# Optimization experiments

Measured on AMD Instinct MI355X. Metric: run time of the kernel, lower is better.

The kernel has to match this reference:

```python
import jax, jax.numpy as jnp
import numpy as np
from jax import lax


def _conv2d(x, w, b, stride):
    # x: [B,C,H,W], w: [O,I,kh,kw], b: [O]
    y = lax.conv_general_dilated(
        x, w, window_strides=(stride, stride), padding='VALID',
        dimension_numbers=('NCHW', 'OIHW', 'NCHW'))
    return y + b[None, :, None, None]


def setup_inputs() -> dict:
    key = jax.random.key(0)
    ks = jax.random.split(key, 4)
    B, C, H, W = 8, 128, 128, 128
    x = jax.random.normal(ks[0], (B, C, H, W), dtype=jnp.float32)
    # conv weights, scaled like torch default init (~1/sqrt(fan_in))
    Wq = jax.random.normal(ks[1], (C, C, 2, 2), dtype=jnp.float32) / np.sqrt(C * 4)
    Wk = jax.random.normal(ks[2], (C, C, 2, 2), dtype=jnp.float32) / np.sqrt(C * 4)
    Wv = jax.random.normal(ks[3], (C, C, 1, 1), dtype=jnp.float32) / np.sqrt(C)
    bq = jnp.zeros((C,), dtype=jnp.float32)
    bk = jnp.zeros((C,), dtype=jnp.float32)
    bv = jnp.zeros((C,), dtype=jnp.float32)
    return {'x': x, 'Wq': Wq, 'bq': bq, 'Wk': Wk, 'bk': bk, 'Wv': Wv, 'bv': bv}


def reference(x, Wq, bq, Wk, bk, Wv, bv):
    B, C, H, W = x.shape
    # query/key: 2x2 stride-2 convs -> [B, C, (H//2)*(W//2)]
    q = _conv2d(x, Wq, bq, 2).reshape(B, C, -1)
    k = _conv2d(x, Wk, bk, 2).reshape(B, C, -1)
    # value: 1x1 conv -> [B, C, H*W]
    v = _conv2d(x, Wv, bv, 1).reshape(B, C, -1)
    # energy: [B, C, C]
    energy = jnp.einsum('bcn,bdn->bcd', q, k)
    # max-subtract trick: softmax over (row_max - energy)
    energy_new = jnp.max(energy, axis=-1, keepdims=True) - energy
    attention = jax.nn.softmax(energy_new, axis=-1)
    out = jnp.einsum('bcd,bdn->bcn', attention, v)
    return out.reshape(B, C, H, W)
```

## Files before the change

kernel.cpp:

```cpp
#include <hip/hip_runtime.h>
#include <math.h>


typedef float f32x4 __attribute__((ext_vector_type(4)));
typedef short s16x8 __attribute__((ext_vector_type(8)));

__device__ __forceinline__ unsigned short f2bf(float f) {
  union { float f; unsigned u; } v; v.f = f;
  unsigned r = v.u + 0x7FFFu + ((v.u >> 16) & 1u);
  return (unsigned short)(r >> 16);
}
__device__ __forceinline__ float bf2f(unsigned short h) {
  union { unsigned u; float f; } v; v.u = ((unsigned)h) << 16;
  return v.f;
}
__device__ __forceinline__ unsigned pack2(unsigned short a, unsigned short b) {
  return (unsigned)a | ((unsigned)b << 16);
}

__global__ __launch_bounds__(256) void k_prep(
    const float* __restrict__ Wq, const float* __restrict__ Wk,
    unsigned short* __restrict__ Wth, unsigned short* __restrict__ Wtl) {
  const int f = (blockIdx.x * 256 + threadIdx.x) * 4;
  const int row = f >> 9;
  const int k   = f & 511;
  const float* src = (row < 128) ? &Wq[row * 512 + k] : &Wk[(row - 128) * 512 + k];
  float4 v = *(const float4*)src;
  unsigned short h0 = f2bf(v.x), h1 = f2bf(v.y), h2 = f2bf(v.z), h3 = f2bf(v.w);
  unsigned short l0 = f2bf(v.x - bf2f(h0)), l1 = f2bf(v.y - bf2f(h1));
  unsigned short l2 = f2bf(v.z - bf2f(h2)), l3 = f2bf(v.w - bf2f(h3));
  const int di = (k >> 5) * 8192 + row * 32 + (k & 31);
  *(ushort4*)&Wth[di] = make_ushort4(h0, h1, h2, h3);
  *(ushort4*)&Wtl[di] = make_ushort4(l0, l1, l2, l3);
}

__global__ __launch_bounds__(256, 3) void k_conv_energy(
    const float* __restrict__ x,
    const unsigned short* __restrict__ Wth, const unsigned short* __restrict__ Wtl,
    const float* __restrict__ bq, const float* __restrict__ bk,
    float* __restrict__ epart) {
  __shared__ unsigned short LDS[16384];
  unsigned short* Th = LDS;
  unsigned short* Tl = LDS + 8192;

  const int t = threadIdx.x;
  const int nt = blockIdx.x, b = blockIdx.y;
  const int w = t >> 6, lane = t & 63;
  const int lrow = lane & 15, lkb = lane >> 4;

  const int pp = t >> 4;
  const int ci_l = pp >> 1, kh = pp & 1;
  const int i16 = t & 15;
  const int klb = ci_l * 4 + kh * 2;
  const float* xb = x + ((size_t)b << 21);
  const float* xrow = xb + (size_t)ci_l * 16384 + (2 * nt + kh) * 128 + 2 * i16;

  f32x4 acc[4][4];
#pragma unroll
  for (int m = 0; m < 4; ++m)
#pragma unroll
    for (int n = 0; n < 4; ++n) acc[m][n] = (f32x4){0.f, 0.f, 0.f, 0.f};

  s16x8 pfh[4], pfl[4];
  float2 pv[2][4];
  const int aoff = (w * 64 + lrow) * 32 + lkb * 8;

#pragma unroll
  for (int m = 0; m < 4; ++m) {
    pfh[m] = *(const s16x8*)&Wth[aoff + m * 512];
    pfl[m] = *(const s16x8*)&Wtl[aoff + m * 512];
  }
  {
    float2 v0 = *(const float2*)&xrow[0];
    float2 v1 = *(const float2*)&xrow[32];
    float2 v2 = *(const float2*)&xrow[64];
    float2 v3 = *(const float2*)&xrow[96];
    unsigned short hx, hy;
    hx = f2bf(v0.x); hy = f2bf(v0.y);
    *(unsigned*)&LDS[(i16     ) * 40 + klb] = pack2(hx, hy);
    *(unsigned*)&LDS[2560 + (i16     ) * 40 + klb] = pack2(f2bf(v0.x - bf2f(hx)), f2bf(v0.y - bf2f(hy)));
    hx = f2bf(v1.x); hy = f2bf(v1.y);
    *(unsigned*)&LDS[(i16 + 16) * 40 + klb] = pack2(hx, hy);
    *(unsigned*)&LDS[2560 + (i16 + 16) * 40 + klb] = pack2(f2bf(v1.x - bf2f(hx)), f2bf(v1.y - bf2f(hy)));
    hx = f2bf(v2.x); hy = f2bf(v2.y);
    *(unsigned*)&LDS[(i16 + 32) * 40 + klb] = pack2(hx, hy);
    *(unsigned*)&LDS[2560 + (i16 + 32) * 40 + klb] = pack2(f2bf(v2.x - bf2f(hx)), f2bf(v2.y - bf2f(hy)));
    hx = f2bf(v3.x); hy = f2bf(v3.y);
    *(unsigned*)&LDS[(i16 + 48) * 40 + klb] = pack2(hx, hy);
    *(unsigned*)&LDS[2560 + (i16 + 48) * 40 + klb] = pack2(f2bf(v3.x - bf2f(hx)), f2bf(v3.y - bf2f(hy)));
  }
#pragma unroll
  for (int g = 0; g < 4; ++g)
    pv[1][g] = *(const float2*)&xrow[(size_t)8 * 16384 + 32 * g];
  __syncthreads();

#pragma unroll
  for (int step = 0; step < 16; ++step) {
    const int cur = step & 1;
    const unsigned short* Bh = LDS + cur * 5120;
    const unsigned short* Bl = Bh + 2560;
    s16x8 bfh[4], bfl[4];
#pragma unroll
    for (int nf = 0; nf < 4; ++nf) {
      const int bidx = (nf * 16 + lrow) * 40 + lkb * 8;
      bfh[nf] = *(const s16x8*)&Bh[bidx];
      bfl[nf] = *(const s16x8*)&Bl[bidx];
    }
#pragma unroll
    for (int m = 0; m < 4; ++m)
#pragma unroll
      for (int n = 0; n < 4; ++n) {
        acc[m][n] = __builtin_amdgcn_mfma_f32_16x16x32_bf16(pfh[m], bfh[n], acc[m][n], 0, 0, 0);
        acc[m][n] = __builtin_amdgcn_mfma_f32_16x16x32_bf16(pfh[m], bfl[n], acc[m][n], 0, 0, 0);
        acc[m][n] = __builtin_amdgcn_mfma_f32_16x16x32_bf16(pfl[m], bfh[n], acc[m][n], 0, 0, 0);
      }
    if (step < 15) {
      const unsigned short* Wh_n = Wth + (step + 1) * 8192;
      const unsigned short* Wl_n = Wtl + (step + 1) * 8192;
#pragma unroll
      for (int m = 0; m < 4; ++m) {
        pfh[m] = *(const s16x8*)&Wh_n[aoff + m * 512];
        pfl[m] = *(const s16x8*)&Wl_n[aoff + m * 512];
      }
    }
    if (step < 14) {
#pragma unroll
      for (int g = 0; g < 4; ++g)
        pv[cur][g] = *(const float2*)&xrow[(size_t)(step + 2) * 8 * 16384 + 32 * g];
    }
    if (step < 15) {
      unsigned short* Nh = LDS + (cur ^ 1) * 5120;
      unsigned short* Nl = Nh + 2560;
#pragma unroll
      for (int g = 0; g < 4; ++g) {
        const int n = i16 + 16 * g;
        unsigned short hx = f2bf(pv[cur ^ 1][g].x), hy = f2bf(pv[cur ^ 1][g].y);
        *(unsigned*)&Nh[n * 40 + klb] = pack2(hx, hy);
        *(unsigned*)&Nl[n * 40 + klb] = pack2(f2bf(pv[cur ^ 1][g].x - bf2f(hx)),
                                              f2bf(pv[cur ^ 1][g].y - bf2f(hy)));
      }
      asm volatile("s_waitcnt lgkmcnt(0)" ::: "memory");
      __builtin_amdgcn_s_barrier();
    }
  }
  __syncthreads();

  const float* biasp = (w < 2) ? bq : bk;
  const int rb = (w & 1) * 64;
  float biasr[16];
#pragma unroll
  for (int m = 0; m < 4; ++m)
#pragma unroll
    for (int i = 0; i < 4; ++i)
      biasr[m * 4 + i] = biasp[rb + m * 16 + (lane >> 4) * 4 + i];

  f32x4 e[4][4];
#pragma unroll
  for (int m = 0; m < 4; ++m)
#pragma unroll
    for (int n = 0; n < 4; ++n) e[m][n] = (f32x4){0.f, 0.f, 0.f, 0.f};

  const int mrow0 = (w >> 1) * 64;
  const int nrow0 = 128 + (w & 1) * 64;

#pragma unroll
  for (int ks = 0; ks < 2; ++ks) {
#pragma unroll
    for (int m = 0; m < 4; ++m) {
      const int r0 = w * 64 + m * 16 + (lane >> 4) * 4;
#pragma unroll
      for (int nn = 0; nn < 2; ++nn) {
        const int n = 2 * ks + nn;
        const int cl = nn * 16 + lrow;
        const int cl8 = cl >> 3, c7 = cl & 7;
#pragma unroll
        for (int i = 0; i < 4; ++i) {
          const int r = r0 + i;
          const float vv = acc[m][n][i] + biasr[m * 4 + i];
          const unsigned short h = f2bf(vv);
          const unsigned short l = f2bf(vv - bf2f(h));
          const int ad = r * 32 + ((cl8 ^ (r & 3)) << 3) + c7;
          Th[ad] = h;
          Tl[ad] = l;
        }
      }
    }
    __syncthreads();
    {
      s16x8 qh[4], ql[4], kh8[4], kl8[4];
#pragma unroll
      for (int m = 0; m < 4; ++m) {
        const int r = mrow0 + m * 16 + lrow;
        const int ad = r * 32 + ((lkb ^ (r & 3)) << 3);
        qh[m] = *(const s16x8*)&Th[ad];
        ql[m] = *(const s16x8*)&Tl[ad];
      }
#pragma unroll
      for (int n = 0; n < 4; ++n) {
        const int r = nrow0 + n * 16 + lrow;
        const int ad = r * 32 + ((lkb ^ (r & 3)) << 3);
        kh8[n] = *(const s16x8*)&Th[ad];
        kl8[n] = *(const s16x8*)&Tl[ad];
      }
#pragma unroll
      for (int m = 0; m < 4; ++m)
#pragma unroll
        for (int n = 0; n < 4; ++n) {
          e[m][n] = __builtin_amdgcn_mfma_f32_16x16x32_bf16(qh[m], kh8[n], e[m][n], 0, 0, 0);
          e[m][n] = __builtin_amdgcn_mfma_f32_16x16x32_bf16(qh[m], kl8[n], e[m][n], 0, 0, 0);
          e[m][n] = __builtin_amdgcn_mfma_f32_16x16x32_bf16(ql[m], kh8[n], e[m][n], 0, 0, 0);
        }
    }
    if (ks == 0) __syncthreads();
  }

  float* ep = epart + ((size_t)b * 64 + nt) * 16384;
#pragma unroll
  for (int m = 0; m < 4; ++m) {
    const int qr = (w >> 1) * 64 + m * 16 + (lane >> 4) * 4;
#pragma unroll
    for (int n = 0; n < 4; ++n) {
      const int kr = (w & 1) * 64 + n * 16 + lrow;
#pragma unroll
      for (int i = 0; i < 4; ++i) ep[(size_t)(qr + i) * 128 + kr] = e[m][n][i];
    }
  }
}

__global__ __launch_bounds__(256) void k_softmax_M(
    const float* __restrict__ epart, const float* __restrict__ Wv,
    const float* __restrict__ bv, float* __restrict__ Mbuf,
    float* __restrict__ outbb) {
  __shared__ float As[4][2][128];
  const int t = threadIdx.x;
  const int wid = t >> 6, lane = t & 63;
  const int half = lane >> 5, l32 = lane & 31;
  const int b = blockIdx.x >> 4;
  const int c = (blockIdx.x & 15) * 8 + wid * 2 + half;
  const int d0 = l32 * 4;

  float4 s = make_float4(0.f, 0.f, 0.f, 0.f);
#pragma unroll 8
  for (int p = 0; p < 64; ++p) {
    float4 e = *(const float4*)&epart[((size_t)b * 64 + p) * 16384 + c * 128 + d0];
    s.x += e.x; s.y += e.y; s.z += e.z; s.w += e.w;
  }
  float mn = fminf(fminf(s.x, s.y), fminf(s.z, s.w));
#pragma unroll
  for (int off = 1; off < 32; off <<= 1) mn = fminf(mn, __shfl_xor(mn, off));
  const float p0 = expf(mn - s.x);
  const float p1 = expf(mn - s.y);
  const float p2 = expf(mn - s.z);
  const float p3 = expf(mn - s.w);
  float tot = (p0 + p1) + (p2 + p3);
#pragma unroll
  for (int off = 1; off < 32; off <<= 1) tot += __shfl_xor(tot, off);
  const float inv = 1.f / tot;
  const float a0 = p0 * inv, a1 = p1 * inv, a2 = p2 * inv, a3 = p3 * inv;

  const float4 bvv = *(const float4*)&bv[d0];
  float ob = a0 * bvv.x + a1 * bvv.y + a2 * bvv.z + a3 * bvv.w;
#pragma unroll
  for (int off = 1; off < 32; off <<= 1) ob += __shfl_xor(ob, off);
  if (l32 == 0) outbb[b * 128 + c] = ob;

  *(float4*)&As[wid][half][d0] = make_float4(a0, a1, a2, a3);
  float4 m = make_float4(0.f, 0.f, 0.f, 0.f);
#pragma unroll 4
  for (int d = 0; d < 128; ++d) {
    const float a = As[wid][half][d];
    const float4 wv = *(const float4*)&Wv[d * 128 + d0];
    m.x = fmaf(a, wv.x, m.x);
    m.y = fmaf(a, wv.y, m.y);
    m.z = fmaf(a, wv.z, m.z);
    m.w = fmaf(a, wv.w, m.w);
  }
  *(float4*)&Mbuf[(size_t)b * 16384 + c * 128 + d0] = m;
}

__global__ __launch_bounds__(256) void k_out(
    const float* __restrict__ x, const float* __restrict__ Mbuf,
    const float* __restrict__ outbb, float* __restrict__ out) {
  __shared__ unsigned short Ms[128 * 40];
  __shared__ unsigned short Xs[128 * 40];
  const int t = threadIdx.x;
  const int nt = blockIdx.x, b = blockIdx.y;
  const int wid = t >> 6, lane = t & 63;
  const int wr = wid >> 1, wc = wid & 1;
  const int lrow = lane & 15, lkb = lane >> 4;
  const int am = t >> 1, ak0 = (t & 1) * 16;
  const int xkl = (t >> 5) * 4;
  const int xc0 = (t & 31) * 4;

  const float* xb = x + ((size_t)b << 21);
  const float* Mb = Mbuf + (size_t)b * 16384;
  float* ob = out + ((size_t)b << 21);

  f32x4 acc[4][4];
#pragma unroll
  for (int m = 0; m < 4; ++m)
#pragma unroll
    for (int n = 0; n < 4; ++n) acc[m][n] = (f32x4){0.f, 0.f, 0.f, 0.f};

  for (int step = 0; step < 4; ++step) {
    const int kk = step * 32;
    {
      float w[16];
      *(float4*)&w[0]  = *(const float4*)&Mb[am * 128 + kk + ak0];
      *(float4*)&w[4]  = *(const float4*)&Mb[am * 128 + kk + ak0 + 4];
      *(float4*)&w[8]  = *(const float4*)&Mb[am * 128 + kk + ak0 + 8];
      *(float4*)&w[12] = *(const float4*)&Mb[am * 128 + kk + ak0 + 12];
      unsigned short hs[16];
#pragma unroll
      for (int i = 0; i < 16; ++i) hs[i] = f2bf(w[i]);
      *(uint4*)&Ms[am * 40 + ak0]     = *(uint4*)&hs[0];
      *(uint4*)&Ms[am * 40 + ak0 + 8] = *(uint4*)&hs[8];
    }
#pragma unroll
    for (int q = 0; q < 4; ++q) {
      const int kl = xkl + q;
      float4 v = *(const float4*)&xb[(size_t)(kk + kl) * 16384 + nt * 128 + xc0];
      Xs[(xc0 + 0) * 40 + kl] = f2bf(v.x);
      Xs[(xc0 + 1) * 40 + kl] = f2bf(v.y);
      Xs[(xc0 + 2) * 40 + kl] = f2bf(v.z);
      Xs[(xc0 + 3) * 40 + kl] = f2bf(v.w);
    }
    __syncthreads();
    s16x8 af[4], bf[4];
#pragma unroll
    for (int m = 0; m < 4; ++m)
      af[m] = *(const s16x8*)&Ms[(wr * 64 + m * 16 + lrow) * 40 + lkb * 8];
#pragma unroll
    for (int n = 0; n < 4; ++n)
      bf[n] = *(const s16x8*)&Xs[(wc * 64 + n * 16 + lrow) * 40 + lkb * 8];
#pragma unroll
    for (int m = 0; m < 4; ++m)
#pragma unroll
      for (int n = 0; n < 4; ++n)
        acc[m][n] = __builtin_amdgcn_mfma_f32_16x16x32_bf16(af[m], bf[n], acc[m][n], 0, 0, 0);
    __syncthreads();
  }
#pragma unroll
  for (int m = 0; m < 4; ++m) {
    const int r0 = wr * 64 + m * 16 + (lane >> 4) * 4;
#pragma unroll
    for (int n = 0; n < 4; ++n) {
      const int gc = nt * 128 + wc * 64 + n * 16 + (lane & 15);
#pragma unroll
      for (int i = 0; i < 4; ++i) {
        const int row = r0 + i;
        ob[(size_t)row * 16384 + gc] = acc[m][n][i] + outbb[b * 128 + row];
      }
    }
  }
}

extern "C" void kernel_launch(void* const* d_in, const int* in_sizes, int n_in,
                              void* d_out, int out_size, void* d_ws, size_t ws_size,
                              hipStream_t stream) {
  const float* x  = (const float*)d_in[0];
  const float* Wq = (const float*)d_in[1];
  const float* bq = (const float*)d_in[2];
  const float* Wk = (const float*)d_in[3];
  const float* bk = (const float*)d_in[4];
  const float* Wv = (const float*)d_in[5];
  const float* bv = (const float*)d_in[6];
  float* out = (float*)d_out;
  char* ws = (char*)d_ws;

  float* epart = (float*)ws;
  float* Mbuf  = (float*)(ws + 33554432);
  float* outbb = (float*)(ws + 34078720);
  unsigned short* Wth = (unsigned short*)(ws + 34082816);
  unsigned short* Wtl = (unsigned short*)(ws + 34344960);

  hipLaunchKernelGGL(k_prep, dim3(128), dim3(256), 0, stream, Wq, Wk, Wth, Wtl);
  hipLaunchKernelGGL(k_conv_energy, dim3(64, 8), dim3(256), 0, stream,
                     x, Wth, Wtl, bq, bk, epart);
  hipLaunchKernelGGL(k_softmax_M, dim3(128), dim3(256), 0, stream,
                     epart, Wv, bv, Mbuf, outbb);
  hipLaunchKernelGGL(k_out, dim3(128, 8), dim3(256), 0, stream,
                     x, Mbuf, outbb, out);
}
```

Before: 84.23 us.

## Split conv-energy work across 512 threads with smaller per-wave tiles

```diff
diff --git a/kernel.cpp b/kernel.cpp
--- a/kernel.cpp
+++ b/kernel.cpp
@@ -34,7 +34,7 @@
   *(ushort4*)&Wtl[di] = make_ushort4(l0, l1, l2, l3);
 }
 
-__global__ __launch_bounds__(256, 3) void k_conv_energy(
+__global__ __launch_bounds__(512, 4) void k_conv_energy(
     const float* __restrict__ x,
     const unsigned short* __restrict__ Wth, const unsigned short* __restrict__ Wtl,
     const float* __restrict__ bq, const float* __restrict__ bk,
@@ -48,50 +48,43 @@
   const int w = t >> 6, lane = t & 63;
   const int lrow = lane & 15, lkb = lane >> 4;
 
-  const int pp = t >> 4;
-  const int ci_l = pp >> 1, kh = pp & 1;
-  const int i16 = t & 15;
+  const int ci_l = w;
+  const int kh = (t >> 5) & 1;
+  const int i32 = t & 31;
   const int klb = ci_l * 4 + kh * 2;
   const float* xb = x + ((size_t)b << 21);
-  const float* xrow = xb + (size_t)ci_l * 16384 + (2 * nt + kh) * 128 + 2 * i16;
-
-  f32x4 acc[4][4];
-#pragma unroll
-  for (int m = 0; m < 4; ++m)
+  const float* xrow = xb + (size_t)ci_l * 16384 + (2 * nt + kh) * 128 + 2 * i32;
+
+  f32x4 acc[2][4];
+#pragma unroll
+  for (int m = 0; m < 2; ++m)
 #pragma unroll
     for (int n = 0; n < 4; ++n) acc[m][n] = (f32x4){0.f, 0.f, 0.f, 0.f};
 
-  s16x8 pfh[4], pfl[4];
-  float2 pv[2][4];
-  const int aoff = (w * 64 + lrow) * 32 + lkb * 8;
-
-#pragma unroll
-  for (int m = 0; m < 4; ++m) {
+  s16x8 pfh[2], pfl[2];
+  float2 pv[2][2];
+  const int aoff = (w * 32 + lrow) * 32 + lkb * 8;
+
+#pragma unroll
+  for (int m = 0; m < 2; ++m) {
     pfh[m] = *(const s16x8*)&Wth[aoff + m * 512];
     pfl[m] = *(const s16x8*)&Wtl[aoff + m * 512];
   }
   {
     float2 v0 = *(const float2*)&xrow[0];
-    float2 v1 = *(const float2*)&xrow[32];
-    float2 v2 = *(const float2*)&xrow[64];
-    float2 v3 = *(const float2*)&xrow[96];
+    float2 v1 = *(const float2*)&xrow[64];
     unsigned short hx, hy;
     hx = f2bf(v0.x); hy = f2bf(v0.y);
-    *(unsigned*)&LDS[(i16     ) * 40 + klb] = pack2(hx, hy);
-    *(unsigned*)&LDS[2560 + (i16     ) * 40 + klb] = pack2(f2bf(v0.x - bf2f(hx)), f2bf(v0.y - bf2f(hy)));
+    *(unsigned*)&LDS[i32 * 40 + klb] = pack2(hx, hy);
+    *(unsigned*)&LDS[2560 + i32 * 40 + klb] =
+        pack2(f2bf(v0.x - bf2f(hx)), f2bf(v0.y - bf2f(hy)));
     hx = f2bf(v1.x); hy = f2bf(v1.y);
-    *(unsigned*)&LDS[(i16 + 16) * 40 + klb] = pack2(hx, hy);
-    *(unsigned*)&LDS[2560 + (i16 + 16) * 40 + klb] = pack2(f2bf(v1.x - bf2f(hx)), f2bf(v1.y - bf2f(hy)));
-    hx = f2bf(v2.x); hy = f2bf(v2.y);
-    *(unsigned*)&LDS[(i16 + 32) * 40 + klb] = pack2(hx, hy);
-    *(unsigned*)&LDS[2560 + (i16 + 32) * 40 + klb] = pack2(f2bf(v2.x - bf2f(hx)), f2bf(v2.y - bf2f(hy)));
-    hx = f2bf(v3.x); hy = f2bf(v3.y);
-    *(unsigned*)&LDS[(i16 + 48) * 40 + klb] = pack2(hx, hy);
-    *(unsigned*)&LDS[2560 + (i16 + 48) * 40 + klb] = pack2(f2bf(v3.x - bf2f(hx)), f2bf(v3.y - bf2f(hy)));
-  }
-#pragma unroll
-  for (int g = 0; g < 4; ++g)
-    pv[1][g] = *(const float2*)&xrow[(size_t)8 * 16384 + 32 * g];
+    *(unsigned*)&LDS[(i32 + 32) * 40 + klb] = pack2(hx, hy);
+    *(unsigned*)&LDS[2560 + (i32 + 32) * 40 + klb] =
+        pack2(f2bf(v1.x - bf2f(hx)), f2bf(v1.y - bf2f(hy)));
+  }
+  pv[1][0] = *(const float2*)&xrow[(size_t)8 * 16384];
+  pv[1][1] = *(const float2*)&xrow[(size_t)8 * 16384 + 64];
   __syncthreads();
 
 #pragma unroll
@@ -107,7 +100,7 @@
       bfl[nf] = *(const s16x8*)&Bl[bidx];
     }
 #pragma unroll
-    for (int m = 0; m < 4; ++m)
+    for (int m = 0; m < 2; ++m)
 #pragma unroll
       for (int n = 0; n < 4; ++n) {
         acc[m][n] = __builtin_amdgcn_mfma_f32_16x16x32_bf16(pfh[m], bfh[n], acc[m][n], 0, 0, 0);
@@ -118,56 +111,51 @@
       const unsigned short* Wh_n = Wth + (step + 1) * 8192;
       const unsigned short* Wl_n = Wtl + (step + 1) * 8192;
 #pragma unroll
-      for (int m = 0; m < 4; ++m) {
+      for (int m = 0; m < 2; ++m) {
         pfh[m] = *(const s16x8*)&Wh_n[aoff + m * 512];
         pfl[m] = *(const s16x8*)&Wl_n[aoff + m * 512];
       }
     }
     if (step < 14) {
-#pragma unroll
-      for (int g = 0; g < 4; ++g)
-        pv[cur][g] = *(const float2*)&xrow[(size_t)(step + 2) * 8 * 16384 + 32 * g];
+      pv[cur][0] = *(const float2*)&xrow[(size_t)(step + 2) * 8 * 16384];
+      pv[cur][1] = *(const float2*)&xrow[(size_t)(step + 2) * 8 * 16384 + 64];
     }
     if (step < 15) {
       unsigned short* Nh = LDS + (cur ^ 1) * 5120;
       unsigned short* Nl = Nh + 2560;
-#pragma unroll
-      for (int g = 0; g < 4; ++g) {
-        const int n = i16 + 16 * g;
-        unsigned short hx = f2bf(pv[cur ^ 1][g].x), hy = f2bf(pv[cur ^ 1][g].y);
-        *(unsigned*)&Nh[n * 40 + klb] = pack2(hx, hy);
-        *(unsigned*)&Nl[n * 40 + klb] = pack2(f2bf(pv[cur ^ 1][g].x - bf2f(hx)),
-                                              f2bf(pv[cur ^ 1][g].y - bf2f(hy)));
-      }
+      unsigned short hx, hy;
+      hx = f2bf(pv[cur ^ 1][0].x); hy = f2bf(pv[cur ^ 1][0].y);
+      *(unsigned*)&Nh[i32 * 40 + klb] = pack2(hx, hy);
+      *(unsigned*)&Nl[i32 * 40 + klb] =
+          pack2(f2bf(pv[cur ^ 1][0].x - bf2f(hx)), f2bf(pv[cur ^ 1][0].y - bf2f(hy)));
+      hx = f2bf(pv[cur ^ 1][1].x); hy = f2bf(pv[cur ^ 1][1].y);
+      *(unsigned*)&Nh[(i32 + 32) * 40 + klb] = pack2(hx, hy);
+      *(unsigned*)&Nl[(i32 + 32) * 40 + klb] =
+          pack2(f2bf(pv[cur ^ 1][1].x - bf2f(hx)), f2bf(pv[cur ^ 1][1].y - bf2f(hy)));
       asm volatile("s_waitcnt lgkmcnt(0)" ::: "memory");
       __builtin_amdgcn_s_barrier();
     }
   }
   __syncthreads();
 
-  const float* biasp = (w < 2) ? bq : bk;
-  const int rb = (w & 1) * 64;
-  float biasr[16];
-#pragma unroll
-  for (int m = 0; m < 4; ++m)
+  const float* biasp = (w < 4) ? bq : bk;
+  const int rb = (w & 3) * 32;
+  float biasr[8];
+#pragma unroll
+  for (int m = 0; m < 2; ++m)
 #pragma unroll
     for (int i = 0; i < 4; ++i)
       biasr[m * 4 + i] = biasp[rb + m * 16 + (lane >> 4) * 4 + i];
 
-  f32x4 e[4][4];
-#pragma unroll
-  for (int m = 0; m < 4; ++m)
-#pragma unroll
-    for (int n = 0; n < 4; ++n) e[m][n] = (f32x4){0.f, 0.f, 0.f, 0.f};
-
-  const int mrow0 = (w >> 1) * 64;
-  const int nrow0 = 128 + (w & 1) * 64;
+  f32x4 e[8];
+#pragma unroll
+  for (int n = 0; n < 8; ++n) e[n] = (f32x4){0.f, 0.f, 0.f, 0.f};
 
 #pragma unroll
   for (int ks = 0; ks < 2; ++ks) {
 #pragma unroll
-    for (int m = 0; m < 4; ++m) {
-      const int r0 = w * 64 + m * 16 + (lane >> 4) * 4;
+    for (int m = 0; m < 2; ++m) {
+      const int r0 = w * 32 + m * 16 + (lane >> 4) * 4;
 #pragma unroll
       for (int nn = 0; nn < 2; ++nn) {
         const int n = 2 * ks + nn;
@@ -187,42 +175,42 @@
     }
     __syncthreads();
     {
-      s16x8 qh[4], ql[4], kh8[4], kl8[4];
-#pragma unroll
-      for (int m = 0; m < 4; ++m) {
-        const int r = mrow0 + m * 16 + lrow;
+      s16x8 qh, ql;
+      {
+        const int r = w * 16 + lrow;
         const int ad = r * 32 + ((lkb ^ (r & 3)) << 3);
-        qh[m] = *(const s16x8*)&Th[ad];
-        ql[m] = *(const s16x8*)&Tl[ad];
-      }
-#pragma unroll
-      for (int n = 0; n < 4; ++n) {
-        const int r = nrow0 + n * 16 + lrow;
-        const int ad = r * 32 + ((lkb ^ (r & 3)) << 3);
-        kh8[n] = *(const s16x8*)&Th[ad];
-        kl8[n] = *(const s16x8*)&Tl[ad];
-      }
-#pragma unroll
-      for (int m = 0; m < 4; ++m)
-#pragma unroll
-        for (int n = 0; n < 4; ++n) {
-          e[m][n] = __builtin_amdgcn_mfma_f32_16x16x32_bf16(qh[m], kh8[n], e[m][n], 0, 0, 0);
-          e[m][n] = __builtin_amdgcn_mfma_f32_16x16x32_bf16(qh[m], kl8[n], e[m][n], 0, 0, 0);
-          e[m][n] = __builtin_amdgcn_mfma_f32_16x16x32_bf16(ql[m], kh8[n], e[m][n], 0, 0, 0);
+        qh = *(const s16x8*)&Th[ad];
+        ql = *(const s16x8*)&Tl[ad];
+      }
+#pragma unroll
+      for (int g = 0; g < 2; ++g) {
+        s16x8 kh8[4], kl8[4];
+#pragma unroll
+        for (int j = 0; j < 4; ++j) {
+          const int r = 128 + (g * 4 + j) * 16 + lrow;
+          const int ad = r * 32 + ((lkb ^ (r & 3)) << 3);
+          kh8[j] = *(const s16x8*)&Th[ad];
+          kl8[j] = *(const s16x8*)&Tl[ad];
         }
+#pragma unroll
+        for (int j = 0; j < 4; ++j) {
+          e[g * 4 + j] = __builtin_amdgcn_mfma_f32_16x16x32_bf16(qh, kh8[j], e[g * 4 + j], 0, 0, 0);
+          e[g * 4 + j] = __builtin_amdgcn_mfma_f32_16x16x32_bf16(qh, kl8[j], e[g * 4 + j], 0, 0, 0);
+          e[g * 4 + j] = __builtin_amdgcn_mfma_f32_16x16x32_bf16(ql, kh8[j], e[g * 4 + j], 0, 0, 0);
+        }
+      }
     }
     if (ks == 0) __syncthreads();
   }
 
   float* ep = epart + ((size_t)b * 64 + nt) * 16384;
 #pragma unroll
-  for (int m = 0; m < 4; ++m) {
-    const int qr = (w >> 1) * 64 + m * 16 + (lane >> 4) * 4;
-#pragma unroll
-    for (int n = 0; n < 4; ++n) {
-      const int kr = (w & 1) * 64 + n * 16 + lrow;
-#pragma unroll
-      for (int i = 0; i < 4; ++i) ep[(size_t)(qr + i) * 128 + kr] = e[m][n][i];
+  for (int n = 0; n < 8; ++n) {
+    const int kr = n * 16 + (lane & 15);
+#pragma unroll
+    for (int i = 0; i < 4; ++i) {
+      const int qr = w * 16 + (lane >> 4) * 4 + i;
+      ep[(size_t)qr * 128 + kr] = e[n][i];
     }
   }
 }
@@ -375,7 +363,7 @@
   unsigned short* Wtl = (unsigned short*)(ws + 34344960);
 
   hipLaunchKernelGGL(k_prep, dim3(128), dim3(256), 0, stream, Wq, Wk, Wth, Wtl);
-  hipLaunchKernelGGL(k_conv_energy, dim3(64, 8), dim3(256), 0, stream,
+  hipLaunchKernelGGL(k_conv_energy, dim3(64, 8), dim3(512), 0, stream,
                      x, Wth, Wtl, bq, bk, epart);
   hipLaunchKernelGGL(k_softmax_M, dim3(128), dim3(256), 0, stream,
                      epart, Wv, bv, Mbuf, outbb);
```

After: 87.04 us. +3.3%, slower.
